# Performance work log

Hardware: AMD Instinct MI355X
Metric: run time of the kernel (lower is better)

The kernel has to match this reference:

```python
import jax, jax.numpy as jnp
import numpy as np

OS_FACTOR = 1.5

def setup_inputs() -> dict:
    key = jax.random.key(0)
    k = jax.random.split(key, 5)
    B, T, I, H = 64, 1024, 1024, 1024
    s = 1.0 / np.sqrt(H).astype(np.float32)
    return {
        "x": jax.random.normal(k[0], (B, T, I), dtype=jnp.float32),
        "W_ih": jax.random.normal(k[1], (H, I), dtype=jnp.float32) * s,
        "W_hh": jax.random.normal(k[2], (H, H), dtype=jnp.float32) * s,
        "b_ih": jax.random.normal(k[3], (H,), dtype=jnp.float32) * s,
        "b_hh": jax.random.normal(k[4], (H,), dtype=jnp.float32) * s,
    }

def reference(x, W_ih, W_hh, b_ih, b_hh):
    B, T, I = x.shape
    H = W_hh.shape[0]
    delay_near = int(np.floor(OS_FACTOR))   # 1
    delay_far = int(np.ceil(OS_FACTOR))     # 2
    alpha = jnp.float32(OS_FACTOR - delay_near)  # 0.5
    # Precompute input projection for all steps (same math, batched GEMM): [T,B,H]
    xw = jnp.einsum('bti,hi->tbh', x, W_ih) + b_ih + b_hh
    # Circular delay buffer of the last `delay_far` states, zero-initialized.
    # In the torch code, negative indices into the zero `states` buffer read zeros,
    # which matches a zero-initialized buffer here.
    buf0 = jnp.zeros((delay_far, B, H), dtype=x.dtype)

    def step(buf, xw_t):
        # buf[-1] = state at t-1, buf[0] = state at t-delay_far
        h_read = (1.0 - alpha) * buf[delay_far - delay_near] + alpha * buf[0]
        h = jnp.tanh(xw_t + h_read @ W_hh.T)
        buf = jnp.concatenate([buf[1:], h[None]], axis=0)
        return buf, h

    _, states = jax.lax.scan(step, buf0, xw)   # states: [T,B,H]
    states = jnp.swapaxes(states, 0, 1)        # [B,T,H]
    h_final = states[:, -1, :][None]           # [1,B,H]
    return states, h_final
```

## Files before the change

kernel.cpp:

```cpp
#include <hip/hip_runtime.h>
#include <stdint.h>
#include <stddef.h>

#define TT 1024
#define BB 64
#define HH 1024
#define II 1024

typedef __attribute__((ext_vector_type(8))) short s16x8;
typedef __attribute__((ext_vector_type(4))) float f32x4;
typedef __attribute__((ext_vector_type(2))) unsigned u32x2;

#define WS_RING  4096

static __device__ __forceinline__ unsigned cvtpk(float lo, float hi) {
    unsigned r;
    asm("v_cvt_pk_bf16_f32 %0, %1, %2" : "=v"(r) : "v"(lo), "v"(hi));
    return r;
}

static __device__ __forceinline__ s16x8 pack8(float4 a, float4 b) {
    union { unsigned u[4]; s16x8 v; } r;
    r.u[0] = cvtpk(a.x, a.y);
    r.u[1] = cvtpk(a.z, a.w);
    r.u[2] = cvtpk(b.x, b.y);
    r.u[3] = cvtpk(b.z, b.w);
    return r.v;
}

static __device__ __forceinline__ f32x4 zero4() {
    f32x4 v = {0.f, 0.f, 0.f, 0.f};
    return v;
}

static __device__ __forceinline__ s16x8 ld16_sc01(const void* p) {
    s16x8 v;
    asm volatile("global_load_dwordx4 %0, %1, off sc0 sc1" : "=v"(v) : "v"(p));
    return v;
}
static __device__ __forceinline__ unsigned ld4_sc01_wait(const void* p) {
    unsigned v;
    asm volatile("global_load_dword %0, %1, off sc0 sc1\n\ts_waitcnt vmcnt(0)"
                 : "=v"(v) : "v"(p) : "memory");
    return v;
}
static __device__ __forceinline__ void st8_sc01(void* p, u32x2 v) {
    asm volatile("global_store_dwordx2 %0, %1, off sc0 sc1" :: "v"(p), "v"(v) : "memory");
}
#define WAITV(n) do { asm volatile("s_waitcnt vmcnt(" #n ")" ::: "memory"); \
                      __builtin_amdgcn_sched_barrier(0); } while (0)

__global__ void init_ws(unsigned int* w) {
    for (int i = threadIdx.x; i < 1024; i += 256)
        __hip_atomic_store(&w[i], 0u, __ATOMIC_RELAXED, __HIP_MEMORY_SCOPE_AGENT);
}

__global__ __launch_bounds__(256, 3) void xw_gemm(
    const float* __restrict__ X,
    const float* __restrict__ Wih,
    const float* __restrict__ bih,
    const float* __restrict__ bhh,
    float* __restrict__ out)
{
    __shared__ unsigned short As[128 * 64];
    __shared__ unsigned short Bs[128 * 64];

    const int tid  = threadIdx.x;
    const int lane = tid & 63;
    const int wid  = tid >> 6;
    const int L  = blockIdx.x;
    const int bm = (L & 7) * 64 + (L >> 6);
    const int bn = (L >> 3) & 7;
    const size_t m0 = (size_t)bm * 128;
    const int n0 = bn * 128;
    const int wm = (wid >> 1) * 64;
    const int wn = (wid & 1) * 64;

    f32x4 acc[4][4];
#pragma unroll
    for (int i = 0; i < 4; ++i)
#pragma unroll
        for (int jj = 0; jj < 4; ++jj) acc[i][jj] = zero4();

    const int srow  = tid >> 1;
    const int shalf = tid & 1;
    const float* xp = X   + (m0 + srow) * (size_t)II + shalf * 32;
    const float* wp = Wih + (size_t)(n0 + srow) * II + shalf * 32;

    for (int kt = 0; kt < II / 64; ++kt) {
#pragma unroll
        for (int i = 0; i < 4; ++i) {
            float4 a0 = *(const float4*)(xp + i * 8);
            float4 a1 = *(const float4*)(xp + i * 8 + 4);
            float4 b0 = *(const float4*)(wp + i * 8);
            float4 b1 = *(const float4*)(wp + i * 8 + 4);
            const int c = shalf * 4 + i;
            const int cw = (c ^ (srow & 7)) << 3;
            *(s16x8*)&As[srow * 64 + cw] = pack8(a0, a1);
            *(s16x8*)&Bs[srow * 64 + cw] = pack8(b0, b1);
        }
        __syncthreads();

#pragma unroll
        for (int kk = 0; kk < 2; ++kk) {
            s16x8 af[4], bf[4];
            const int cs = kk * 4 + (lane >> 4);
#pragma unroll
            for (int mi = 0; mi < 4; ++mi) {
                const int r = wm + mi * 16 + (lane & 15);
                af[mi] = *(const s16x8*)&As[r * 64 + ((cs ^ (r & 7)) << 3)];
            }
#pragma unroll
            for (int ni = 0; ni < 4; ++ni) {
                const int r = wn + ni * 16 + (lane & 15);
                bf[ni] = *(const s16x8*)&Bs[r * 64 + ((cs ^ (r & 7)) << 3)];
            }
#pragma unroll
            for (int mi = 0; mi < 4; ++mi)
#pragma unroll
                for (int ni = 0; ni < 4; ++ni)
                    acc[mi][ni] = __builtin_amdgcn_mfma_f32_16x16x32_bf16(
                        af[mi], bf[ni], acc[mi][ni], 0, 0, 0);
        }
        __syncthreads();
        xp += 64; wp += 64;
    }

#pragma unroll
    for (int ni = 0; ni < 4; ++ni) {
        const int col = n0 + wn + ni * 16 + (lane & 15);
        const float bias = bih[col] + bhh[col];
#pragma unroll
        for (int mi = 0; mi < 4; ++mi) {
            const size_t row = m0 + wm + mi * 16 + ((lane >> 4) << 2);
#pragma unroll
            for (int r = 0; r < 4; ++r)
                out[(row + r) * (size_t)HH + col] = acc[mi][ni][r] + bias;
        }
    }
}

__global__ __launch_bounds__(256, 1) void rnn_scan(
    const float* __restrict__ Whh,
    float* __restrict__ out,
    void* __restrict__ ws)
{
    __shared__ unsigned short Hl[8 * 1024];

    const int tid  = threadIdx.x;
    const int lane = tid & 63;
    const int wid  = tid >> 6;
    const int g  = blockIdx.x >> 4;
    const int sl = blockIdx.x & 15;

    const int jb = sl * 64 + wid * 16;
    const int kg = lane >> 4;

    s16x8 afr[32];
    {
        const float* wr = Whh + (size_t)(jb + (lane & 15)) * HH + kg * 8;
#pragma unroll
        for (int c = 0; c < 32; ++c) {
            float4 p0 = *(const float4*)(wr + c * 32);
            float4 p1 = *(const float4*)(wr + c * 32 + 4);
            afr[c] = pack8(p0, p1);
        }
    }

    unsigned* fl = (unsigned*)ws + g * 128;
    unsigned* myflag = fl + sl * 8;
    char* rg = (char*)ws + WS_RING + (size_t)g * 32768;

    const int srow = tid >> 5;
    const int sseg = tid & 31;
    const char* sbase0 = rg + srow * 2048 + sseg * 16;
    const char* sbase1 = sbase0 + 16384;

    const int bl   = lane & 15;
    const int blv  = bl & 7;
    const int act  = bl < 8;
    const int b    = g * 8 + blv;
    const int f0   = jb + kg * 4;
    const int hrow = blv;

    float hprev[4];

    {
        const size_t idx = ((size_t)b * TT) * HH + f0;
        float4 xw4 = *(const float4*)(out + idx);
        float4 st;
        st.x = tanhf(xw4.x); st.y = tanhf(xw4.y);
        st.z = tanhf(xw4.z); st.w = tanhf(xw4.w);
        hprev[0] = st.x; hprev[1] = st.y; hprev[2] = st.z; hprev[3] = st.w;
        if (act) {
            u32x2 pk;
            pk[0] = cvtpk(0.5f * st.x, 0.5f * st.y);
            pk[1] = cvtpk(0.5f * st.z, 0.5f * st.w);
            st8_sc01(rg + 16384 + blv * 2048 + f0 * 2, pk);
        }
        asm volatile("s_waitcnt vmcnt(0)" ::: "memory");
        __syncthreads();
        if (tid == 0)
            __hip_atomic_store(myflag, 1u, __ATOMIC_RELAXED,
                               __HIP_MEMORY_SCOPE_AGENT);
        if (act) *(float4*)(out + idx) = st;
    }

#pragma unroll 1
    for (int t = 1; t < TT; ++t) {
        const size_t xidx = ((size_t)b * TT + t) * HH + f0;
        float4 xw4 = *(const float4*)(out + xidx);

        {
            const unsigned* myp = fl + (lane & 15) * 8;
            for (;;) {
                unsigned v = ld4_sc01_wait(myp);
                if (__all((int)(v >= (unsigned)t))) break;
                __builtin_amdgcn_s_sleep(1);
            }
            asm volatile("" ::: "memory");
            __builtin_amdgcn_sched_barrier(0);
        }

        {
            const char* sp = (t & 1) ? sbase1 : sbase0;
            s16x8 v[4];
#pragma unroll
            for (int i = 0; i < 4; ++i) v[i] = ld16_sc01(sp + i * 512);
#pragma unroll
            for (int i = 0; i < 4; ++i) {
                if (i == 0)      { WAITV(3); }
                else if (i == 1) { WAITV(2); }
                else if (i == 2) { WAITV(1); }
                else             { WAITV(0); }
                const int c = sseg + i * 32;
                *(s16x8*)&Hl[srow * 1024 + ((c ^ (srow & 7)) << 3)] = v[i];
            }
        }
        __syncthreads();

        f32x4 acc[4];
#pragma unroll
        for (int i = 0; i < 4; ++i) acc[i] = zero4();
#pragma unroll
        for (int kb = 0; kb < 4; ++kb) {
            s16x8 h8[8];
#pragma unroll
            for (int ki = 0; ki < 8; ++ki) {
                const int cs = (kb * 8 + ki) * 4 + kg;
                h8[ki] = *(const s16x8*)&Hl[hrow * 1024 + ((cs ^ (hrow & 7)) << 3)];
            }
#pragma unroll
            for (int ki = 0; ki < 8; ++ki)
                acc[ki & 3] = __builtin_amdgcn_mfma_f32_16x16x32_bf16(
                    afr[kb * 8 + ki], h8[ki], acc[ki & 3], 0, 0, 0);
        }
        f32x4 accT = acc[0] + acc[1] + acc[2] + acc[3];

        {
            float hn[4];
#pragma unroll
            for (int r = 0; r < 4; ++r)
                hn[r] = tanhf(accT[r] + ((const float*)&xw4)[r]);
            float4 st; st.x = hn[0]; st.y = hn[1]; st.z = hn[2]; st.w = hn[3];
            if (t < TT - 1) {
                if (act) {
                    u32x2 pk;
                    pk[0] = cvtpk(0.5f * (hn[0] + hprev[0]),
                                  0.5f * (hn[1] + hprev[1]));
                    pk[1] = cvtpk(0.5f * (hn[2] + hprev[2]),
                                  0.5f * (hn[3] + hprev[3]));
                    char* rw = rg + (size_t)((t + 1) & 1) * 16384;
                    st8_sc01(rw + blv * 2048 + f0 * 2, pk);
                }
                asm volatile("s_waitcnt vmcnt(0)" ::: "memory");
                __syncthreads();
                if (tid == 0)
                    __hip_atomic_store(myflag, (unsigned)(t + 1),
                                       __ATOMIC_RELAXED, __HIP_MEMORY_SCOPE_AGENT);
                if (act) *(float4*)(out + xidx) = st;
            } else {
                if (act) {
                    *(float4*)(out + xidx) = st;
                    *(float4*)(out + (size_t)BB * TT * HH + (size_t)b * HH + f0) = st;
                }
            }
#pragma unroll
            for (int r = 0; r < 4; ++r) hprev[r] = hn[r];
        }
    }
}

extern "C" void kernel_launch(void* const* d_in, const int* in_sizes, int n_in,
                              void* d_out, int out_size, void* d_ws, size_t ws_size,
                              hipStream_t stream)
{
    const float* X   = (const float*)d_in[0];
    const float* Wih = (const float*)d_in[1];
    const float* Whh = (const float*)d_in[2];
    const float* bih = (const float*)d_in[3];
    const float* bhh = (const float*)d_in[4];
    float* out = (float*)d_out;

    init_ws<<<dim3(1), dim3(256), 0, stream>>>((unsigned int*)d_ws);
    xw_gemm<<<dim3(4096), dim3(256), 0, stream>>>(X, Wih, bih, bhh, out);
    rnn_scan<<<dim3(128), dim3(256), 0, stream>>>(Whh, out, d_ws);
}
```

Baseline: 3.460 ms.

## Double-buffer LDS tiles in xw_gemm to overlap global loads with MFMA

The input-projection GEMM now keeps two LDS buffers for the A and B tiles. The next k-tile's global loads are issued into registers before the current tile's MFMA work, then converted and written to the alternate buffer afterwards, so only one barrier is needed per iteration. This is meant to hide global load latency behind compute. In exchange it doubles LDS use and lowers the occupancy hint from 3 to 2 blocks per CU, and it keeps 16 float4 values live in registers.

```diff
diff --git a/kernel.cpp b/kernel.cpp
--- a/kernel.cpp
+++ b/kernel.cpp
@@ -9,6 +9,7 @@
 
 typedef __attribute__((ext_vector_type(8))) short s16x8;
 typedef __attribute__((ext_vector_type(4))) float f32x4;
+typedef __attribute__((ext_vector_type(4))) unsigned u32x4;
 typedef __attribute__((ext_vector_type(2))) unsigned u32x2;
 
 #define WS_RING  4096
@@ -18,14 +19,11 @@
     asm("v_cvt_pk_bf16_f32 %0, %1, %2" : "=v"(r) : "v"(lo), "v"(hi));
     return r;
 }
-
-static __device__ __forceinline__ s16x8 pack8(float4 a, float4 b) {
-    union { unsigned u[4]; s16x8 v; } r;
-    r.u[0] = cvtpk(a.x, a.y);
-    r.u[1] = cvtpk(a.z, a.w);
-    r.u[2] = cvtpk(b.x, b.y);
-    r.u[3] = cvtpk(b.z, b.w);
-    return r.v;
+static __device__ __forceinline__ u32x4 pk4(float4 a, float4 b) {
+    u32x4 r;
+    r[0] = cvtpk(a.x, a.y); r[1] = cvtpk(a.z, a.w);
+    r[2] = cvtpk(b.x, b.y); r[3] = cvtpk(b.z, b.w);
+    return r;
 }
 
 static __device__ __forceinline__ f32x4 zero4() {
@@ -55,15 +53,15 @@
         __hip_atomic_store(&w[i], 0u, __ATOMIC_RELAXED, __HIP_MEMORY_SCOPE_AGENT);
 }
 
-__global__ __launch_bounds__(256, 3) void xw_gemm(
+__global__ __launch_bounds__(256, 2) void xw_gemm(
     const float* __restrict__ X,
     const float* __restrict__ Wih,
     const float* __restrict__ bih,
     const float* __restrict__ bhh,
     float* __restrict__ out)
 {
-    __shared__ unsigned short As[128 * 64];
-    __shared__ unsigned short Bs[128 * 64];
+    __shared__ unsigned short As[2][128 * 64];
+    __shared__ unsigned short Bs[2][128 * 64];
 
     const int tid  = threadIdx.x;
     const int lane = tid & 63;
@@ -87,19 +85,39 @@
     const float* xp = X   + (m0 + srow) * (size_t)II + shalf * 32;
     const float* wp = Wih + (size_t)(n0 + srow) * II + shalf * 32;
 
-    for (int kt = 0; kt < II / 64; ++kt) {
-#pragma unroll
-        for (int i = 0; i < 4; ++i) {
-            float4 a0 = *(const float4*)(xp + i * 8);
-            float4 a1 = *(const float4*)(xp + i * 8 + 4);
-            float4 b0 = *(const float4*)(wp + i * 8);
-            float4 b1 = *(const float4*)(wp + i * 8 + 4);
-            const int c = shalf * 4 + i;
-            const int cw = (c ^ (srow & 7)) << 3;
-            *(s16x8*)&As[srow * 64 + cw] = pack8(a0, a1);
-            *(s16x8*)&Bs[srow * 64 + cw] = pack8(b0, b1);
-        }
-        __syncthreads();
+    float4 a4[8], b4[8];
+
+#pragma unroll
+    for (int i = 0; i < 4; ++i) {
+        a4[2 * i]     = *(const float4*)(xp + i * 8);
+        a4[2 * i + 1] = *(const float4*)(xp + i * 8 + 4);
+        b4[2 * i]     = *(const float4*)(wp + i * 8);
+        b4[2 * i + 1] = *(const float4*)(wp + i * 8 + 4);
+    }
+#pragma unroll
+    for (int i = 0; i < 4; ++i) {
+        const int c = shalf * 4 + i;
+        const int cw = (c ^ (srow & 7)) << 3;
+        *(u32x4*)&As[0][srow * 64 + cw] = pk4(a4[2 * i], a4[2 * i + 1]);
+        *(u32x4*)&Bs[0][srow * 64 + cw] = pk4(b4[2 * i], b4[2 * i + 1]);
+    }
+    __syncthreads();
+
+#pragma unroll 1
+    for (int kt = 0; kt < 16; ++kt) {
+        const int cur = kt & 1, nxt = cur ^ 1;
+
+        if (kt < 15) {
+            xp += 64; wp += 64;
+#pragma unroll
+            for (int i = 0; i < 4; ++i) {
+                a4[2 * i]     = *(const float4*)(xp + i * 8);
+                a4[2 * i + 1] = *(const float4*)(xp + i * 8 + 4);
+                b4[2 * i]     = *(const float4*)(wp + i * 8);
+                b4[2 * i + 1] = *(const float4*)(wp + i * 8 + 4);
+            }
+            __builtin_amdgcn_sched_barrier(0);
+        }
 
 #pragma unroll
         for (int kk = 0; kk < 2; ++kk) {
@@ -108,12 +126,12 @@
 #pragma unroll
             for (int mi = 0; mi < 4; ++mi) {
                 const int r = wm + mi * 16 + (lane & 15);
-                af[mi] = *(const s16x8*)&As[r * 64 + ((cs ^ (r & 7)) << 3)];
+                af[mi] = *(const s16x8*)&As[cur][r * 64 + ((cs ^ (r & 7)) << 3)];
             }
 #pragma unroll
             for (int ni = 0; ni < 4; ++ni) {
                 const int r = wn + ni * 16 + (lane & 15);
-                bf[ni] = *(const s16x8*)&Bs[r * 64 + ((cs ^ (r & 7)) << 3)];
+                bf[ni] = *(const s16x8*)&Bs[cur][r * 64 + ((cs ^ (r & 7)) << 3)];
             }
 #pragma unroll
             for (int mi = 0; mi < 4; ++mi)
@@ -122,8 +140,17 @@
                     acc[mi][ni] = __builtin_amdgcn_mfma_f32_16x16x32_bf16(
                         af[mi], bf[ni], acc[mi][ni], 0, 0, 0);
         }
+
+        if (kt < 15) {
+#pragma unroll
+            for (int i = 0; i < 4; ++i) {
+                const int c = shalf * 4 + i;
+                const int cw = (c ^ (srow & 7)) << 3;
+                *(u32x4*)&As[nxt][srow * 64 + cw] = pk4(a4[2 * i], a4[2 * i + 1]);
+                *(u32x4*)&Bs[nxt][srow * 64 + cw] = pk4(b4[2 * i], b4[2 * i + 1]);
+            }
+        }
         __syncthreads();
-        xp += 64; wp += 64;
     }
 
 #pragma unroll
@@ -163,7 +190,9 @@
         for (int c = 0; c < 32; ++c) {
             float4 p0 = *(const float4*)(wr + c * 32);
             float4 p1 = *(const float4*)(wr + c * 32 + 4);
-            afr[c] = pack8(p0, p1);
+            union { u32x4 u; s16x8 v; } cv;
+            cv.u = pk4(p0, p1);
+            afr[c] = cv.v;
         }
     }
 
```

Measured after the change: 3.366 ms. 1.03x faster.
